# Optimization experiments

Hardware: AMD Instinct MI355X
Metric: run time of the kernel (lower is better)

Reference implementation:

```python
import jax, jax.numpy as jnp
import numpy as np

D_MODEL = 1024
N_HEADS = 16
D_FF = 4096
EPS = 1e-5


def _linear_init(key, fan_in, fan_out):
    # torch nn.Linear default: U(-1/sqrt(fan_in), 1/sqrt(fan_in))
    k1, k2 = jax.random.split(key)
    bound = 1.0 / np.sqrt(fan_in)
    W = jax.random.uniform(k1, (fan_in, fan_out), minval=-bound, maxval=bound, dtype=jnp.float32)
    b = jax.random.uniform(k2, (fan_out,), minval=-bound, maxval=bound, dtype=jnp.float32)
    return W, b


def setup_inputs() -> dict:
    key = jax.random.key(0)
    ks = jax.random.split(key, 8)
    x = jax.random.normal(ks[0], (4, 2048, D_MODEL), dtype=jnp.float32)
    Wq, bq = _linear_init(ks[1], D_MODEL, D_MODEL)
    Wk, bk = _linear_init(ks[2], D_MODEL, D_MODEL)
    Wv, bv = _linear_init(ks[3], D_MODEL, D_MODEL)
    Wo, bo = _linear_init(ks[4], D_MODEL, D_MODEL)
    W1, b1 = _linear_init(ks[5], D_MODEL, D_FF)
    W2, b2 = _linear_init(ks[6], D_FF, D_MODEL)
    g1 = jnp.ones((D_MODEL,), jnp.float32); be1 = jnp.zeros((D_MODEL,), jnp.float32)
    g2 = jnp.ones((D_MODEL,), jnp.float32); be2 = jnp.zeros((D_MODEL,), jnp.float32)
    return {"x": x, "Wq": Wq, "bq": bq, "Wk": Wk, "bk": bk, "Wv": Wv, "bv": bv,
            "Wo": Wo, "bo": bo, "g1": g1, "be1": be1, "W1": W1, "b1": b1,
            "W2": W2, "b2": b2, "g2": g2, "be2": be2}


def _layernorm(x, g, b):
    mu = jnp.mean(x, axis=-1, keepdims=True)
    var = jnp.mean(jnp.square(x - mu), axis=-1, keepdims=True)
    return (x - mu) * jax.lax.rsqrt(var + EPS) * g + b


def reference(x, Wq, bq, Wk, bk, Wv, bv, Wo, bo, g1, be1, W1, b1, W2, b2, g2, be2):
    B, T, D = x.shape
    H, dk = N_HEADS, D // N_HEADS
    # projections -> [B, H, T, dk]
    def split_heads(y):
        return y.reshape(B, T, H, dk).transpose(0, 2, 1, 3)
    Q = split_heads(x @ Wq + bq)
    K = split_heads(x @ Wk + bk)
    V = split_heads(x @ Wv + bv)
    scores = jnp.einsum('bhtd,bhsd->bhts', Q, K) / jnp.sqrt(jnp.float32(dk))
    weights = jax.nn.softmax(scores, axis=-1)  # no causal mask in original
    ctx = jnp.einsum('bhts,bhsd->bhtd', weights, V)
    ctx = ctx.transpose(0, 2, 1, 3).reshape(B, T, D)
    attn_out = ctx @ Wo + bo
    x = _layernorm(x + attn_out, g1, be1)
    ff = jax.nn.relu(x @ W1 + b1) @ W2 + b2
    x = _layernorm(x + ff, g2, be2)
    return x
```

## Files before the change

kernel.cpp:

```cpp
#include <hip/hip_runtime.h>
#include <hip/hip_bf16.h>
#include <stdint.h>

typedef __attribute__((ext_vector_type(8))) short short8;
typedef __attribute__((ext_vector_type(4))) float f32x4;
typedef __attribute__((ext_vector_type(16))) float f32x16;

#define SEQ 2048
#define DMODEL 1024
#define NH 16
#define DKH 64

__device__ __forceinline__ uint16_t f2b(float f) {
  uint32_t u = __float_as_uint(f);
  uint32_t r = (u + 0x7fff + ((u >> 16) & 1)) >> 16;
  return (uint16_t)r;
}

__device__ __forceinline__ void gload16(const uint16_t* g, uint16_t* l) {
  __builtin_amdgcn_global_load_lds((const __attribute__((address_space(1))) void*)g,
                                   (__attribute__((address_space(3))) void*)l, 16, 0, 0);
}

__global__ __launch_bounds__(256) void k_castx(const float* __restrict__ x,
                                               uint16_t* __restrict__ xb) {
  int i = blockIdx.x * 256 + threadIdx.x;
  float4 v = reinterpret_cast<const float4*>(x)[i];
  uint16_t o[4] = {f2b(v.x), f2b(v.y), f2b(v.z), f2b(v.w)};
  reinterpret_cast<uint2*>(xb)[i] = *reinterpret_cast<uint2*>(o);
}

__global__ __launch_bounds__(256) void k_tcast(const float* __restrict__ W,
                                               uint16_t* __restrict__ Wt, int K, int N) {
  __shared__ float tile[32][33];
  int n0 = blockIdx.x * 32, k0 = blockIdx.y * 32;
  int tx = threadIdx.x & 31, ty = threadIdx.x >> 5;
#pragma unroll
  for (int i = 0; i < 32; i += 8)
    tile[ty + i][tx] = W[(size_t)(k0 + ty + i) * N + n0 + tx];
  __syncthreads();
#pragma unroll
  for (int i = 0; i < 32; i += 8)
    Wt[(size_t)(n0 + ty + i) * K + k0 + tx] = f2b(tile[tx][ty + i]);
}

__global__ __launch_bounds__(256) void k_vtrans(const uint16_t* __restrict__ V,
                                                uint16_t* __restrict__ Vt) {
  __shared__ uint16_t tile[64][72];
  const int s0 = blockIdx.x * 64;
  const uint16_t* Vp = V + (size_t)blockIdx.y * SEQ * DKH;
  uint16_t* Vtp = Vt + (size_t)blockIdx.y * SEQ * DKH;
  const int t = threadIdx.x;
#pragma unroll
  for (int i = t; i < 512; i += 256) {
    int r = i >> 3, c8 = (i & 7) << 3;
    *reinterpret_cast<uint4*>(&tile[r][c8]) =
        *reinterpret_cast<const uint4*>(Vp + (size_t)(s0 + r) * DKH + c8);
  }
  __syncthreads();
#pragma unroll
  for (int i = t; i < 512; i += 256) {
    int d = i >> 3, s8 = (i & 7) << 3;
    uint16_t tmp[8];
#pragma unroll
    for (int j = 0; j < 8; ++j) tmp[j] = tile[s8 + j][d];
    *reinterpret_cast<uint4*>(Vtp + (size_t)d * SEQ + s0 + s8) = *reinterpret_cast<uint4*>(tmp);
  }
}

#define MODE_QKV 0
#define MODE_RAW 1
#define MODE_RELU 2

template <int BN, int MODE>
__global__ __launch_bounds__(512, 2) void k_gemm2(
    const uint16_t* __restrict__ A, const uint16_t* __restrict__ Bt, int M, int N, int K,
    int nx, const float* __restrict__ bias0, const float* __restrict__ bias1,
    const float* __restrict__ bias2, uint16_t* __restrict__ ob0, uint16_t* __restrict__ ob1,
    uint16_t* __restrict__ ob2, float* __restrict__ of) {
  constexpr int ASZ = 256 * 64;
  constexpr int BSZ = BN * 64;
  __shared__ __align__(16) uint16_t lds[2 * (ASZ + BSZ)];
  uint16_t* const Abase = lds;
  uint16_t* const Bbase = lds + 2 * ASZ;
  constexpr int WN = (BN == 256) ? 4 : 2;
  constexpr int MREP = (BN == 256) ? 8 : 4;
  constexpr int NPH = (BN == 256) ? 4 : 2;
  const int o = blockIdx.x;
  const int chunk = gridDim.x >> 3;
  const int wg = (o & 7) * chunk + (o >> 3);
  const int brow = (wg / nx) << 8;
  const int bcol = (wg % nx) * BN;
  const int t = threadIdx.x;
  const int wid = t >> 6, l = t & 63, g = l >> 4, lr = l & 15;
  const int wr = wid / WN, wc = wid % WN;
  const int wrow = wr * (MREP * 16);
  const int wcol = wc * 64;

  const int srow = t >> 3;
  const int ss0 = (t & 7) ^ (srow & 7);
  const int ss1 = (t & 7) ^ ((srow + 64) & 7);

  auto stage_half = [&](const uint16_t* gsrc, int grow0, int kk, uint16_t* ldst) {
    gload16(gsrc + (size_t)(grow0 + srow) * K + kk + ss0 * 8, ldst + t * 8);
    gload16(gsrc + (size_t)(grow0 + srow + 64) * K + kk + ss1 * 8, ldst + 4096 + t * 8);
  };
  auto rdfrag = [&](const uint16_t* buf, int ar, int kk) -> short8 {
    int slot = ((kk << 2) + g) ^ (ar & 7);
    return *reinterpret_cast<const short8*>(buf + ar * 64 + slot * 8);
  };

  f32x4 acc[MREP][4] = {};
  const int nt = K >> 6;

  stage_half(A, brow, 0, Abase);
  stage_half(A, brow + 128, 0, Abase + 8192);
  stage_half(Bt, bcol, 0, Bbase);
  if (BN == 256) stage_half(Bt, bcol + 128, 0, Bbase + 8192);
  __syncthreads();

  for (int kt = 0; kt < nt; ++kt) {
    const int cur = kt & 1;
    const uint16_t* Ac = Abase + cur * ASZ;
    const uint16_t* Bc = Bbase + cur * BSZ;
    uint16_t* An = Abase + (cur ^ 1) * ASZ;
    uint16_t* Bn = Bbase + (cur ^ 1) * BSZ;
    const bool pf = (kt + 1 < nt);
    const int knx = (kt + 1) << 6;
#pragma unroll
    for (int q = 0; q < NPH; ++q) {
      const int mq = (BN == 256) ? (q >> 1) : 0;
      const int nq = (BN == 256) ? (q & 1) : q;
      short8 af[4][2], bf[2][2];
#pragma unroll
      for (int j = 0; j < 4; ++j)
#pragma unroll
        for (int kk = 0; kk < 2; ++kk)
          af[j][kk] = rdfrag(Ac, wrow + (mq * 4 + j) * 16 + lr, kk);
#pragma unroll
      for (int j = 0; j < 2; ++j)
#pragma unroll
        for (int kk = 0; kk < 2; ++kk)
          bf[j][kk] = rdfrag(Bc, wcol + (nq * 2 + j) * 16 + lr, kk);
      if (pf) {
        if (q == 0) {
          stage_half(A, brow, knx, An);
          stage_half(A, brow + 128, knx, An + 8192);
          if (BN == 128) stage_half(Bt, bcol, knx, Bn);
        }
        if (BN == 256 && q == 1) stage_half(Bt, bcol, knx, Bn);
        if (BN == 256 && q == 2) stage_half(Bt, bcol + 128, knx, Bn + 8192);
      }
      __builtin_amdgcn_s_barrier();
      __builtin_amdgcn_s_setprio(1);
#pragma unroll
      for (int j = 0; j < 4; ++j)
#pragma unroll
        for (int j2 = 0; j2 < 2; ++j2)
#pragma unroll
          for (int kk = 0; kk < 2; ++kk)
            acc[mq * 4 + j][nq * 2 + j2] = __builtin_amdgcn_mfma_f32_16x16x32_bf16(
                af[j][kk], bf[j2][kk], acc[mq * 4 + j][nq * 2 + j2], 0, 0, 0);
      __builtin_amdgcn_s_setprio(0);
      if (q == NPH - 1) {
        asm volatile("s_waitcnt vmcnt(0)" ::: "memory");
        __builtin_amdgcn_s_barrier();
        __builtin_amdgcn_sched_barrier(0);
      } else {
        __builtin_amdgcn_s_barrier();
      }
    }
  }

#pragma unroll
  for (int m = 0; m < MREP; ++m) {
#pragma unroll
    for (int n = 0; n < 4; ++n) {
#pragma unroll
      for (int qi = 0; qi < 4; ++qi) {
        int r = brow + wrow + m * 16 + g * 4 + qi;
        int c = bcol + wcol + n * 16 + lr;
        float v = acc[m][n][qi];
        if (MODE == MODE_QKV) {
          int which = c >> 10;
          int hd = c & 1023;
          const float* bp = which == 0 ? bias0 : (which == 1 ? bias1 : bias2);
          v += bp[hd];
          if (which == 0) v *= 0.1803368801f;
          uint16_t* dst = which == 0 ? ob0 : (which == 1 ? ob1 : ob2);
          int b = r >> 11, tt = r & 2047;
          int h = hd >> 6, d = hd & 63;
          dst[((size_t)((b * NH + h) * SEQ + tt)) * DKH + d] = f2b(v);
        } else if (MODE == MODE_RELU) {
          v += bias0[c];
          v = fmaxf(v, 0.0f);
          ob0[(size_t)r * N + c] = f2b(v);
        } else {
          of[(size_t)r * N + c] = v;
        }
      }
    }
  }
}

__global__ __launch_bounds__(256) void k_attn(const uint16_t* __restrict__ Qb,
                                              const uint16_t* __restrict__ Kb,
                                              const uint16_t* __restrict__ Vtg,
                                              uint16_t* __restrict__ ctx) {
  __shared__ __align__(16) uint16_t Ks[2][64 * 64];
  __shared__ __align__(16) uint16_t Vs[2][64 * 64];
  __shared__ float l_arr[4][32];
  const int o = blockIdx.x;
  const int wg = (o & 7) * 128 + (o >> 3);
  const int qt = wg & 15;
  const int bh = wg >> 4;
  const int b = bh >> 4, h = bh & 15;
  const uint16_t* Qp = Qb + (size_t)bh * SEQ * DKH;
  const uint16_t* Kp = Kb + (size_t)bh * SEQ * DKH;
  const uint16_t* Vp = Vtg + (size_t)bh * SEQ * DKH;
  const int t = threadIdx.x, w = t >> 6, l = t & 63;
  const int lo5 = l & 31, hh = l >> 5;
  const int qbase = qt * 128 + w * 32;

  short8 qf[4];
#pragma unroll
  for (int kc = 0; kc < 4; ++kc)
    qf[kc] = *reinterpret_cast<const short8*>(Qp + (size_t)(qbase + lo5) * DKH + kc * 16 + hh * 8);

  f32x16 oacc[2] = {};
  float lsum = 0.f;

  const int swz = ((l & 7) ^ ((l >> 3) & 7)) << 3;
  const int ci0 = w * 2, ci1 = w * 2 + 1;
  const int r0 = ci0 * 8 + (l >> 3), r1 = ci1 * 8 + (l >> 3);
  uint16_t* ldsK0 = &Ks[0][0] + ci0 * 512 + l * 8;
  uint16_t* ldsK1 = &Ks[0][0] + ci1 * 512 + l * 8;
  uint16_t* ldsV0 = &Vs[0][0] + ci0 * 512 + l * 8;
  uint16_t* ldsV1 = &Vs[0][0] + ci1 * 512 + l * 8;
  const uint16_t* gK0 = Kp + (size_t)r0 * DKH + swz;
  const uint16_t* gK1 = Kp + (size_t)r1 * DKH + swz;
  const uint16_t* gV0 = Vp + (size_t)r0 * SEQ + swz;
  const uint16_t* gV1 = Vp + (size_t)r1 * SEQ + swz;

  gload16(gK0, ldsK0);
  gload16(gK1, ldsK1);
  gload16(gV0, ldsV0);
  gload16(gV1, ldsV1);
  __syncthreads();

  for (int tile = 0; tile < 32; ++tile) {
    const int cur = tile & 1;
    if (tile < 31) {
      const int nxt = (cur ^ 1) * 4096;
      const size_t s0n = (size_t)(tile + 1) * 64;
      gload16(gK0 + s0n * DKH, ldsK0 + nxt);
      gload16(gK1 + s0n * DKH, ldsK1 + nxt);
      gload16(gV0 + s0n, ldsV0 + nxt);
      gload16(gV1 + s0n, ldsV1 + nxt);
    }
    const char* Kbuf = reinterpret_cast<const char*>(&Ks[cur][0]);
    const char* Vbuf = reinterpret_cast<const char*>(&Vs[cur][0]);

#pragma unroll
    for (int sblk = 0; sblk < 2; ++sblk) {
      short8 kf[4];
      const int krow = sblk * 32 + lo5;
      const int kxor = (krow & 7) << 4;
#pragma unroll
      for (int kc = 0; kc < 4; ++kc) {
        int cb = (kc * 32 + hh * 16) ^ kxor;
        kf[kc] = *reinterpret_cast<const short8*>(Kbuf + krow * 128 + cb);
      }
      short8 vf[2][2];
#pragma unroll
      for (int scl = 0; scl < 2; ++scl)
#pragma unroll
        for (int dblk = 0; dblk < 2; ++dblk) {
          int vrow = dblk * 32 + lo5;
          int cb = (sblk * 64 + scl * 32 + hh * 16) ^ ((vrow & 7) << 4);
          vf[scl][dblk] = *reinterpret_cast<const short8*>(Vbuf + vrow * 128 + cb);
        }

      f32x16 sa = {};
      __builtin_amdgcn_s_setprio(1);
#pragma unroll
      for (int kc = 0; kc < 4; ++kc)
        sa = __builtin_amdgcn_mfma_f32_32x32x16_bf16(kf[kc], qf[kc], sa, 0, 0, 0);
      __builtin_amdgcn_s_setprio(0);

      float p[16];
      float ls = 0.f;
#pragma unroll
      for (int r = 0; r < 16; ++r) {
        p[r] = __builtin_amdgcn_exp2f(sa[r]);
        ls += p[r];
      }
      lsum += ls;

      uint32_t clo[4], chi[4];
#pragma unroll
      for (int m = 0; m < 4; ++m) {
        asm("v_cvt_pk_bf16_f32 %0, %1, %2" : "=v"(clo[m]) : "v"(p[4 * m]), "v"(p[4 * m + 1]));
        asm("v_cvt_pk_bf16_f32 %0, %1, %2" : "=v"(chi[m]) : "v"(p[4 * m + 2]), "v"(p[4 * m + 3]));
      }

#pragma unroll
      for (int scl = 0; scl < 2; ++scl) {
        uint32_t a0 = clo[2 * scl], b0 = clo[2 * scl + 1];
        uint32_t a1 = chi[2 * scl], b1 = chi[2 * scl + 1];
        asm("v_permlane32_swap_b32 %0, %1" : "+v"(a0), "+v"(b0));
        asm("v_permlane32_swap_b32 %0, %1" : "+v"(a1), "+v"(b1));
        union {
          uint32_t u[4];
          short8 s;
        } pu;
        pu.u[0] = a0;
        pu.u[1] = a1;
        pu.u[2] = b0;
        pu.u[3] = b1;
        __builtin_amdgcn_s_setprio(1);
#pragma unroll
        for (int dblk = 0; dblk < 2; ++dblk)
          oacc[dblk] = __builtin_amdgcn_mfma_f32_32x32x16_bf16(pu.s, vf[scl][dblk], oacc[dblk], 0, 0, 0);
        __builtin_amdgcn_s_setprio(0);
      }
    }
    __syncthreads();
  }

  {
    float full = lsum + __shfl_xor(lsum, 32, 64);
    if (l < 32) l_arr[w][lo5] = full;
  }
#pragma unroll
  for (int r = 0; r < 16; ++r) {
    int q = (r & 3) + 8 * (r >> 2) + 4 * hh;
    float li = 1.0f / l_arr[w][q];
    int rowg = b * SEQ + qbase + q;
#pragma unroll
    for (int dblk = 0; dblk < 2; ++dblk) {
      int colg = h * DKH + dblk * 32 + lo5;
      ctx[(size_t)rowg * DMODEL + colg] = f2b(oacc[dblk][r] * li);
    }
  }
}

template <bool WRITE_B>
__global__ __launch_bounds__(256) void k_ln(const float* __restrict__ in,
                                            const float* __restrict__ bias,
                                            const float* __restrict__ res,
                                            const float* __restrict__ gam,
                                            const float* __restrict__ bet,
                                            float* __restrict__ outf,
                                            uint16_t* __restrict__ outb) {
  const int row = blockIdx.x;
  const int t = threadIdx.x, lane = t & 63, w = t >> 6;
  float4 v = reinterpret_cast<const float4*>(in + (size_t)row * DMODEL)[t];
  float4 bb0 = reinterpret_cast<const float4*>(bias)[t];
  float4 rr = reinterpret_cast<const float4*>(res + (size_t)row * DMODEL)[t];
  v.x += bb0.x + rr.x;
  v.y += bb0.y + rr.y;
  v.z += bb0.z + rr.z;
  v.w += bb0.w + rr.w;
  float s = v.x + v.y + v.z + v.w;
  float s2 = v.x * v.x + v.y * v.y + v.z * v.z + v.w * v.w;
#pragma unroll
  for (int off = 1; off < 64; off <<= 1) {
    s += __shfl_xor(s, off, 64);
    s2 += __shfl_xor(s2, off, 64);
  }
  __shared__ float rs[4], rq[4];
  if (lane == 0) {
    rs[w] = s;
    rq[w] = s2;
  }
  __syncthreads();
  float ts = rs[0] + rs[1] + rs[2] + rs[3];
  float tq = rq[0] + rq[1] + rq[2] + rq[3];
  const float inv = 1.0f / DMODEL;
  float mu = ts * inv;
  float var = tq * inv - mu * mu;
  float rstd = rsqrtf(var + 1e-5f);
  float4 gg = reinterpret_cast<const float4*>(gam)[t];
  float4 bb = reinterpret_cast<const float4*>(bet)[t];
  float4 y;
  y.x = (v.x - mu) * rstd * gg.x + bb.x;
  y.y = (v.y - mu) * rstd * gg.y + bb.y;
  y.z = (v.z - mu) * rstd * gg.z + bb.z;
  y.w = (v.w - mu) * rstd * gg.w + bb.w;
  reinterpret_cast<float4*>(outf)[(size_t)row * 256 + t] = y;
  if (WRITE_B) {
    uint16_t o[4] = {f2b(y.x), f2b(y.y), f2b(y.z), f2b(y.w)};
    reinterpret_cast<uint2*>(outb)[(size_t)row * 256 + t] = *reinterpret_cast<uint2*>(o);
  }
}

extern "C" void kernel_launch(void* const* d_in, const int* in_sizes, int n_in, void* d_out,
                              int out_size, void* d_ws, size_t ws_size, hipStream_t stream) {
  const float* x = (const float*)d_in[0];
  const float* Wq = (const float*)d_in[1];
  const float* bq = (const float*)d_in[2];
  const float* Wk = (const float*)d_in[3];
  const float* bk = (const float*)d_in[4];
  const float* Wv = (const float*)d_in[5];
  const float* bv = (const float*)d_in[6];
  const float* Wo = (const float*)d_in[7];
  const float* bo = (const float*)d_in[8];
  const float* g1 = (const float*)d_in[9];
  const float* be1 = (const float*)d_in[10];
  const float* W1 = (const float*)d_in[11];
  const float* b1 = (const float*)d_in[12];
  const float* W2 = (const float*)d_in[13];
  const float* b2 = (const float*)d_in[14];
  const float* g2 = (const float*)d_in[15];
  const float* be2 = (const float*)d_in[16];

  char* ws = (char*)d_ws;
  size_t off = 0;
  auto alloc = [&](size_t bytes) {
    char* p = ws + off;
    off += (bytes + 255) & ~(size_t)255;
    return p;
  };
  uint16_t* wt_qkv = (uint16_t*)alloc(3072ull * 1024 * 2);
  uint16_t* wt_o = (uint16_t*)alloc(1024ull * 1024 * 2);
  uint16_t* wt_1 = (uint16_t*)alloc(4096ull * 1024 * 2);
  uint16_t* wt_2 = (uint16_t*)alloc(1024ull * 4096 * 2);
  uint16_t* xb = (uint16_t*)alloc(8192ull * 1024 * 2);
  float* sum1 = (float*)alloc(8192ull * 1024 * 4);
  float* x1f = (float*)alloc(8192ull * 1024 * 4);
  char* big = alloc(16777216ull + 67108864ull);
  uint16_t* Qbuf = (uint16_t*)big;
  uint16_t* Kbuf = (uint16_t*)(big + 16777216ull);
  uint16_t* Vbuf = (uint16_t*)(big + 2 * 16777216ull);
  uint16_t* vt = (uint16_t*)x1f;
  uint16_t* ctx = xb;
  uint16_t* x1b = (uint16_t*)big;
  uint16_t* hbuf = (uint16_t*)(big + 16777216ull);
  (void)ws_size;

  k_tcast<<<dim3(32, 32), 256, 0, stream>>>(Wq, wt_qkv, 1024, 1024);
  k_tcast<<<dim3(32, 32), 256, 0, stream>>>(Wk, wt_qkv + 1024 * 1024, 1024, 1024);
  k_tcast<<<dim3(32, 32), 256, 0, stream>>>(Wv, wt_qkv + 2 * 1024 * 1024, 1024, 1024);
  k_tcast<<<dim3(32, 32), 256, 0, stream>>>(Wo, wt_o, 1024, 1024);
  k_tcast<<<dim3(128, 32), 256, 0, stream>>>(W1, wt_1, 1024, 4096);
  k_tcast<<<dim3(32, 128), 256, 0, stream>>>(W2, wt_2, 4096, 1024);
  k_castx<<<8192, 256, 0, stream>>>(x, xb);
  k_gemm2<256, MODE_QKV><<<384, 512, 0, stream>>>(
      xb, wt_qkv, 8192, 3072, 1024, 12, bq, bk, bv, Qbuf, Kbuf, Vbuf, nullptr);
  k_vtrans<<<dim3(32, 64), 256, 0, stream>>>(Vbuf, vt);
  k_attn<<<1024, 256, 0, stream>>>(Qbuf, Kbuf, vt, ctx);
  k_gemm2<128, MODE_RAW><<<256, 512, 0, stream>>>(
      ctx, wt_o, 8192, 1024, 1024, 8, nullptr, nullptr, nullptr, nullptr, nullptr, nullptr, sum1);
  k_ln<true><<<8192, 256, 0, stream>>>(sum1, bo, x, g1, be1, x1f, x1b);
  k_gemm2<256, MODE_RELU><<<512, 512, 0, stream>>>(
      x1b, wt_1, 8192, 4096, 1024, 16, b1, nullptr, nullptr, hbuf, nullptr, nullptr, nullptr);
  k_gemm2<128, MODE_RAW><<<256, 512, 0, stream>>>(
      hbuf, wt_2, 8192, 1024, 4096, 8, nullptr, nullptr, nullptr, nullptr, nullptr, nullptr, sum1);
  k_ln<false><<<8192, 256, 0, stream>>>(sum1, b2, x1f, g2, be2, (float*)d_out, nullptr);
}
```

Measured before the change: 423.7 us.

## Split GEMM K-tile into two half-stages with finer-grained vmcnt waits

Restructures the bf16 GEMM main loop so each 64-wide K tile is staged and consumed as two 32-wide halves, with a new LDS layout (16-row blocks per wave, XOR swizzle on 4 slots) and matching fragment reads. Instead of waiting for all outstanding global-to-LDS loads at the end of each tile, it waits with a partial vmcnt, so the second half's loads can still be in flight while the first half is consumed. Barriers per phase are reduced accordingly. This is meant to overlap memory latency with MFMA work better. The cost is more intricate synchronisation, with a risk of races if the vmcnt counts are wrong.

Measured after the change: 443.5 us. 4.7% more time.

```diff
diff --git a/kernel.cpp b/kernel.cpp
--- a/kernel.cpp
+++ b/kernel.cpp
@@ -85,7 +85,8 @@
   uint16_t* const Bbase = lds + 2 * ASZ;
   constexpr int WN = (BN == 256) ? 4 : 2;
   constexpr int MREP = (BN == 256) ? 8 : 4;
-  constexpr int NPH = (BN == 256) ? 4 : 2;
+  constexpr int NQ = (BN == 256) ? 4 : 2;
+  constexpr int LHK = (BN == 256) ? 4 : 3;
   const int o = blockIdx.x;
   const int chunk = gridDim.x >> 3;
   const int wg = (o & 7) * chunk + (o >> 3);
@@ -97,27 +98,34 @@
   const int wrow = wr * (MREP * 16);
   const int wcol = wc * 64;
 
-  const int srow = t >> 3;
-  const int ss0 = (t & 7) ^ (srow & 7);
-  const int ss1 = (t & 7) ^ ((srow + 64) & 7);
-
-  auto stage_half = [&](const uint16_t* gsrc, int grow0, int kk, uint16_t* ldst) {
-    gload16(gsrc + (size_t)(grow0 + srow) * K + kk + ss0 * 8, ldst + t * 8);
-    gload16(gsrc + (size_t)(grow0 + srow + 64) * K + kk + ss1 * 8, ldst + 4096 + t * 8);
+  const int srow = (wid << 4) + (l >> 2);
+  const int gg = (l & 3) ^ ((l >> 2) & 3) ^ ((l >> 4) & 1);
+  const int ldso = (wid << 10) + l * 8;
+
+  auto stageA = [&](uint16_t* dst, int kcol, int kk) {
+    gload16(A + (size_t)(brow + srow) * K + kcol + gg * 8, dst + ldso + kk * 512);
+    gload16(A + (size_t)(brow + 128 + srow) * K + kcol + gg * 8, dst + 8192 + ldso + kk * 512);
   };
-  auto rdfrag = [&](const uint16_t* buf, int ar, int kk) -> short8 {
-    int slot = ((kk << 2) + g) ^ (ar & 7);
-    return *reinterpret_cast<const short8*>(buf + ar * 64 + slot * 8);
+  auto stageB = [&](uint16_t* dst, int kcol, int kk) {
+    gload16(Bt + (size_t)(bcol + srow) * K + kcol + gg * 8, dst + ldso + kk * 512);
+    if (BN == 256)
+      gload16(Bt + (size_t)(bcol + 128 + srow) * K + kcol + gg * 8, dst + 8192 + ldso + kk * 512);
+  };
+
+  const int sA = g ^ (lr & 3) ^ ((lr >> 2) & 1);
+  auto rdfrag = [&](const uint16_t* buf, int r16, int kk) -> short8 {
+    return *reinterpret_cast<const short8*>(buf + (r16 << 10) + kk * 512 + (lr << 5) + sA * 8);
   };
 
   f32x4 acc[MREP][4] = {};
   const int nt = K >> 6;
 
-  stage_half(A, brow, 0, Abase);
-  stage_half(A, brow + 128, 0, Abase + 8192);
-  stage_half(Bt, bcol, 0, Bbase);
-  if (BN == 256) stage_half(Bt, bcol + 128, 0, Bbase + 8192);
-  __syncthreads();
+  stageA(Abase, 0, 0);
+  stageB(Bbase, 0, 0);
+  stageA(Abase, 32, 1);
+  stageB(Bbase, 32, 1);
+  asm volatile("s_waitcnt vmcnt(%0)" ::"i"(LHK) : "memory");
+  __builtin_amdgcn_s_barrier();
 
   for (int kt = 0; kt < nt; ++kt) {
     const int cur = kt & 1;
@@ -128,45 +136,37 @@
     const bool pf = (kt + 1 < nt);
     const int knx = (kt + 1) << 6;
 #pragma unroll
-    for (int q = 0; q < NPH; ++q) {
-      const int mq = (BN == 256) ? (q >> 1) : 0;
-      const int nq = (BN == 256) ? (q & 1) : q;
-      short8 af[4][2], bf[2][2];
-#pragma unroll
-      for (int j = 0; j < 4; ++j)
-#pragma unroll
-        for (int kk = 0; kk < 2; ++kk)
-          af[j][kk] = rdfrag(Ac, wrow + (mq * 4 + j) * 16 + lr, kk);
-#pragma unroll
-      for (int j = 0; j < 2; ++j)
-#pragma unroll
-        for (int kk = 0; kk < 2; ++kk)
-          bf[j][kk] = rdfrag(Bc, wcol + (nq * 2 + j) * 16 + lr, kk);
-      if (pf) {
-        if (q == 0) {
-          stage_half(A, brow, knx, An);
-          stage_half(A, brow + 128, knx, An + 8192);
-          if (BN == 128) stage_half(Bt, bcol, knx, Bn);
+    for (int kk = 0; kk < 2; ++kk) {
+#pragma unroll
+      for (int q = 0; q < NQ; ++q) {
+        const int mq = (BN == 256) ? (q >> 1) : 0;
+        const int nq = (BN == 256) ? (q & 1) : q;
+        short8 af[4], bf[2];
+#pragma unroll
+        for (int j = 0; j < 4; ++j) af[j] = rdfrag(Ac, (wrow >> 4) + mq * 4 + j, kk);
+#pragma unroll
+        for (int j = 0; j < 2; ++j) bf[j] = rdfrag(Bc, (wcol >> 4) + nq * 2 + j, kk);
+        if (pf && q == 0) stageA(An, knx + kk * 32, kk);
+        if (pf && q == 1) stageB(Bn, knx + kk * 32, kk);
+        __builtin_amdgcn_s_setprio(1);
+#pragma unroll
+        for (int j = 0; j < 4; ++j)
+#pragma unroll
+          for (int j2 = 0; j2 < 2; ++j2)
+            acc[mq * 4 + j][nq * 2 + j2] = __builtin_amdgcn_mfma_f32_16x16x32_bf16(
+                af[j], bf[j2], acc[mq * 4 + j][nq * 2 + j2], 0, 0, 0);
+        __builtin_amdgcn_s_setprio(0);
+        if (q == NQ - 1) {
+          if (kk == 0) {
+            if (pf)
+              asm volatile("s_waitcnt vmcnt(%0)" ::"i"(LHK) : "memory");
+            else
+              asm volatile("s_waitcnt vmcnt(0)" ::: "memory");
+          } else if (pf) {
+            asm volatile("s_waitcnt vmcnt(%0)" ::"i"(LHK) : "memory");
+          }
+          __builtin_amdgcn_sched_barrier(0);
         }
-        if (BN == 256 && q == 1) stage_half(Bt, bcol, knx, Bn);
-        if (BN == 256 && q == 2) stage_half(Bt, bcol + 128, knx, Bn + 8192);
-      }
-      __builtin_amdgcn_s_barrier();
-      __builtin_amdgcn_s_setprio(1);
-#pragma unroll
-      for (int j = 0; j < 4; ++j)
-#pragma unroll
-        for (int j2 = 0; j2 < 2; ++j2)
-#pragma unroll
-          for (int kk = 0; kk < 2; ++kk)
-            acc[mq * 4 + j][nq * 2 + j2] = __builtin_amdgcn_mfma_f32_16x16x32_bf16(
-                af[j][kk], bf[j2][kk], acc[mq * 4 + j][nq * 2 + j2], 0, 0, 0);
-      __builtin_amdgcn_s_setprio(0);
-      if (q == NPH - 1) {
-        asm volatile("s_waitcnt vmcnt(0)" ::: "memory");
-        __builtin_amdgcn_s_barrier();
-        __builtin_amdgcn_sched_barrier(0);
-      } else {
         __builtin_amdgcn_s_barrier();
       }
     }
```
